# Kernel tuning notes

Hardware: AMD Instinct MI355X
Metric: run time of the kernel (lower is better)

## Reference

```python
import math
import jax, jax.numpy as jnp
import numpy as np

B, H, W = 4, 256, 256
N_PTS = 128
HALF_X = float(W // 2)
HALF_Y = H / 2.0
TWO_PI = 2.0 * math.pi


def fix_radians(tt):
    # faithful to: -relu(-(2*pi - relu(-tt))) + relu(tt)
    relu = jax.nn.relu
    return -relu(-(TWO_PI - relu(-tt))) + relu(tt)


def _pixel_grid():
    # replicate torch's tile/reshape/transpose construction (valid for H == W):
    # y_matrix flat index p -> p mod H ; x_matrix[i, j] = i
    f32 = jnp.float32
    y_flat = jnp.tile(jnp.arange(H, dtype=f32), W)                       # (H*W,)
    x_flat = jnp.tile(jnp.arange(W, dtype=f32), H).reshape(W, H).T.reshape(-1)  # (H*W,)
    return x_flat, y_flat


def _forward(inputs):
    x = inputs[:, :, 0]                                  # (B, N)
    y = inputs[:, :, 1]
    dx, dy = x - HALF_X, y - HALF_Y
    r = jnp.sqrt(dx ** 2 + dy ** 2)                      # (B, N)
    tt = fix_radians(jnp.arctan2(dy, dx))                # (B, N)

    x_flat, y_flat = _pixel_grid()                       # (H*W,)
    gx, gy = x_flat - HALF_X, y_flat - HALF_Y
    r_matrix = jnp.sqrt(gx ** 2 + gy ** 2)               # (H*W,)
    tt_matrix = fix_radians(jnp.arctan2(gy, gx))         # (H*W,)

    # periodic extension of polygon angles/radii: (B, 3N)
    tt1 = jnp.concatenate([tt - TWO_PI, tt, tt + TWO_PI], axis=1)
    r1 = jnp.concatenate([r, r, r], axis=1)

    # RBF angular interpolation: (B, 3N, H*W)
    d = (tt1[:, :, None] - tt_matrix[None, None, :]) ** 2
    d = jnp.minimum(d, 1.0)
    e = jnp.exp(-100.0 * d)
    # weighted radius per pixel, normalized over polygon axis: (B, H*W)
    r_rbf = jnp.einsum('bjp,bj->bp', e, r1) / jnp.sum(e, axis=1)

    flag = jax.nn.relu(1.0 + r_rbf - r_matrix[None, :])  # (B, H*W)
    return flag.reshape(B, H, W)


def setup_inputs() -> dict:
    key = jax.random.key(0)
    inputs = jax.random.uniform(key, (B, N_PTS, 2), dtype=jnp.float32) * float(W)
    return {"inputs": inputs}


def reference(inputs):
    return _forward(inputs)
```

## Files before the change

kernel.cpp:

```cpp
#include <hip/hip_runtime.h>
#include <hip/hip_bf16.h>


#define TWO_PI_F 6.283185307179586f
#define C1_EXP  (-144.26950408889634f)
#define C2_EXP  (72.13475204444817f)

static __device__ __forceinline__ float fast_exp2(float x) {
#if __has_builtin(__builtin_amdgcn_exp2f)
    return __builtin_amdgcn_exp2f(x);
#else
    return exp2f(x);
#endif
}

__global__ __launch_bounds__(384) void fp_prep_kernel(
        const float* __restrict__ in,
        float2* __restrict__ tr,
        float* __restrict__ rbf0)
{
    __shared__ float2 s[384];
    __shared__ float pn[6], pd[6];
    const int b = blockIdx.x;
    const int tid = threadIdx.x;

    if (tid < 128) {
        float x = in[b * 256 + tid * 2 + 0];
        float y = in[b * 256 + tid * 2 + 1];
        float dx = x - 128.0f, dy = y - 128.0f;
        float r = sqrtf(dx * dx + dy * dy);
        float t = fmaxf(atan2f(dy, dx), 0.0f);
        s[tid]       = make_float2(t - TWO_PI_F, r);
        s[tid + 128] = make_float2(t,            r);
        s[tid + 256] = make_float2(t + TWO_PI_F, r);
    }
    __syncthreads();

    tr[b * 384 + tid] = s[tid];

    float2 v = s[tid];
    float d  = fminf(v.x * v.x, 1.0f);
    float e  = fast_exp2(fmaf(d, C1_EXP, C2_EXP));
    float num = e * v.y;
    float den = e;
    #pragma unroll
    for (int off = 32; off > 0; off >>= 1) {
        num += __shfl_down(num, off);
        den += __shfl_down(den, off);
    }
    if ((tid & 63) == 0) { pn[tid >> 6] = num; pd[tid >> 6] = den; }
    __syncthreads();
    if (tid == 0) {
        float n = 0.0f, dd = 0.0f;
        #pragma unroll
        for (int w = 0; w < 6; ++w) { n += pn[w]; dd += pd[w]; }
        rbf0[b] = n / dd;
    }
}

__global__ __launch_bounds__(256) void fp_main_kernel(
        const float2* __restrict__ tr,
        const float* __restrict__ rbf0,
        float* __restrict__ out)
{
    __shared__ float2 s[384];
    const int tid = threadIdx.x;
    const int bid = blockIdx.x;
    const int b = bid >> 8;
    const int i = bid & 255;

    const float2* trb = tr + b * 384;
    s[tid] = trb[tid];
    if (tid < 128) s[tid + 256] = trb[tid + 256];

    float gx = (float)i   - 128.0f;
    float gy = (float)tid - 128.0f;
    float rm  = sqrtf(gx * gx + gy * gy);
    float ttm = fmaxf(atan2f(gy, gx), 0.0f);
    __syncthreads();

    float rbf;
    if (__all(ttm == 0.0f)) {
        rbf = rbf0[b];
    } else {
        float num = 0.0f, den = 0.0f;
        #pragma unroll 8
        for (int jj = 0; jj < 384; ++jj) {
            float2 v = s[jj];
            float dt = v.x - ttm;
            float d  = fminf(dt * dt, 1.0f);
            float e  = fast_exp2(fmaf(d, C1_EXP, C2_EXP));
            num = fmaf(e, v.y, num);
            den += e;
        }
        rbf = num / den;
    }

    out[bid * 256 + tid] = fmaxf(1.0f + rbf - rm, 0.0f);
}

extern "C" void kernel_launch(void* const* d_in, const int* in_sizes, int n_in,
                              void* d_out, int out_size, void* d_ws, size_t ws_size,
                              hipStream_t stream) {
    const float* in = (const float*)d_in[0];
    float* out = (float*)d_out;

    float2* tr  = (float2*)d_ws;
    float* rbf0 = (float*)((char*)d_ws + 4 * 384 * sizeof(float2));

    fp_prep_kernel<<<4, 384, 0, stream>>>(in, tr, rbf0);
    fp_main_kernel<<<1024, 256, 0, stream>>>(tr, rbf0, out);
}
```

Baseline: 66.20 us.

## Fuse prep into main kernel and drop periodic copies via exp floor constant

Merges the prep kernel into the main kernel: each block now recomputes the polygon angles and radii from the input in shared memory, which removes the second launch and the workspace round trip. Because angles are clamped to [0, 2π), the shifted copies at t±2π always have squared distance at least 1 from pixel angles and so contribute the constant floor exp(-100). The loop now covers only the 128 original points and adds that constant analytically. The exchange is redundant per-block atan2/sqrt work and reliance on the clamping invariant for exactness.

```diff
diff --git a/kernel.cpp b/kernel.cpp
--- a/kernel.cpp
+++ b/kernel.cpp
@@ -2,9 +2,9 @@
 #include <hip/hip_bf16.h>
 
 
-#define TWO_PI_F 6.283185307179586f
 #define C1_EXP  (-144.26950408889634f)
 #define C2_EXP  (72.13475204444817f)
+#define FLOOR_E (1.9287498479639178e-22f)
 
 static __device__ __forceinline__ float fast_exp2(float x) {
 #if __has_builtin(__builtin_amdgcn_exp2f)
@@ -14,79 +14,59 @@
 #endif
 }
 
-__global__ __launch_bounds__(384) void fp_prep_kernel(
+__global__ __launch_bounds__(256) void fp_fused_kernel(
         const float* __restrict__ in,
-        float2* __restrict__ tr,
-        float* __restrict__ rbf0)
-{
-    __shared__ float2 s[384];
-    __shared__ float pn[6], pd[6];
-    const int b = blockIdx.x;
-    const int tid = threadIdx.x;
-
-    if (tid < 128) {
-        float x = in[b * 256 + tid * 2 + 0];
-        float y = in[b * 256 + tid * 2 + 1];
-        float dx = x - 128.0f, dy = y - 128.0f;
-        float r = sqrtf(dx * dx + dy * dy);
-        float t = fmaxf(atan2f(dy, dx), 0.0f);
-        s[tid]       = make_float2(t - TWO_PI_F, r);
-        s[tid + 128] = make_float2(t,            r);
-        s[tid + 256] = make_float2(t + TWO_PI_F, r);
-    }
-    __syncthreads();
-
-    tr[b * 384 + tid] = s[tid];
-
-    float2 v = s[tid];
-    float d  = fminf(v.x * v.x, 1.0f);
-    float e  = fast_exp2(fmaf(d, C1_EXP, C2_EXP));
-    float num = e * v.y;
-    float den = e;
-    #pragma unroll
-    for (int off = 32; off > 0; off >>= 1) {
-        num += __shfl_down(num, off);
-        den += __shfl_down(den, off);
-    }
-    if ((tid & 63) == 0) { pn[tid >> 6] = num; pd[tid >> 6] = den; }
-    __syncthreads();
-    if (tid == 0) {
-        float n = 0.0f, dd = 0.0f;
-        #pragma unroll
-        for (int w = 0; w < 6; ++w) { n += pn[w]; dd += pd[w]; }
-        rbf0[b] = n / dd;
-    }
-}
-
-__global__ __launch_bounds__(256) void fp_main_kernel(
-        const float2* __restrict__ tr,
-        const float* __restrict__ rbf0,
         float* __restrict__ out)
 {
-    __shared__ float2 s[384];
+    __shared__ float2 s_tr[128];
+    __shared__ float  s_part[2][3];
     const int tid = threadIdx.x;
     const int bid = blockIdx.x;
     const int b = bid >> 8;
     const int i = bid & 255;
 
-    const float2* trb = tr + b * 384;
-    s[tid] = trb[tid];
-    if (tid < 128) s[tid + 256] = trb[tid + 256];
+    if (tid < 128) {
+        float2 p = ((const float2*)in)[b * 128 + tid];
+        float dx = p.x - 128.0f, dy = p.y - 128.0f;
+        float r = sqrtf(dx * dx + dy * dy);
+        float t = fmaxf(atan2f(dy, dx), 0.0f);
+        s_tr[tid] = make_float2(t, r);
+        float d0 = fminf(t * t, 1.0f);
+        float e0 = fast_exp2(fmaf(d0, C1_EXP, C2_EXP));
+        float er = e0 * r, se = e0, sr = r;
+        #pragma unroll
+        for (int off = 32; off > 0; off >>= 1) {
+            er += __shfl_down(er, off);
+            se += __shfl_down(se, off);
+            sr += __shfl_down(sr, off);
+        }
+        if ((tid & 63) == 0) {
+            s_part[tid >> 6][0] = er;
+            s_part[tid >> 6][1] = se;
+            s_part[tid >> 6][2] = sr;
+        }
+    }
+    __syncthreads();
 
-    float gx = (float)i   - 128.0f;
-    float gy = (float)tid - 128.0f;
-    float rm  = sqrtf(gx * gx + gy * gy);
-    float ttm = fmaxf(atan2f(gy, gx), 0.0f);
-    __syncthreads();
+    const float sumER = s_part[0][0] + s_part[1][0];
+    const float sumE  = s_part[0][1] + s_part[1][1];
+    const float sumR  = s_part[0][2] + s_part[1][2];
+    const float floorNum = 2.0f * sumR * FLOOR_E;
+    const float floorDen = 256.0f * FLOOR_E;
+
+    const float gx = (float)i   - 128.0f;
+    const float gy = (float)tid - 128.0f;
+    const float rm  = sqrtf(gx * gx + gy * gy);
+    const float ttm = fmaxf(atan2f(gy, gx), 0.0f);
 
     float rbf;
     if (__all(ttm == 0.0f)) {
-        rbf = rbf0[b];
+        rbf = (sumER + floorNum) / (sumE + floorDen);
     } else {
-        float num = 0.0f, den = 0.0f;
+        float num = floorNum, den = floorDen;
         #pragma unroll 8
-        for (int jj = 0; jj < 384; ++jj) {
-            float2 v = s[jj];
+        for (int jj = 0; jj < 128; ++jj) {
+            float2 v = s_tr[jj];
             float dt = v.x - ttm;
             float d  = fminf(dt * dt, 1.0f);
             float e  = fast_exp2(fmaf(d, C1_EXP, C2_EXP));
@@ -104,10 +84,5 @@
                               hipStream_t stream) {
     const float* in = (const float*)d_in[0];
     float* out = (float*)d_out;
-
-    float2* tr  = (float2*)d_ws;
-    float* rbf0 = (float*)((char*)d_ws + 4 * 384 * sizeof(float2));
-
-    fp_prep_kernel<<<4, 384, 0, stream>>>(in, tr, rbf0);
-    fp_main_kernel<<<1024, 256, 0, stream>>>(tr, rbf0, out);
+    fp_fused_kernel<<<1024, 256, 0, stream>>>(in, out);
 }
```

Result: faster. 57.09 us (-13.8%).
